# Kernel optimization log

Hardware: AMD Instinct MI355X
Metric: run time of the kernel (lower is better)

## Reference

```python
import jax, jax.numpy as jnp
import numpy as np

B, S, H, NH = 2, 2048, 2048, 16
HD = H // NH  # 128
NEG = -1e9


def _rope_tables(seq_len, dim, dtype):
    inv_freq = 1.0 / (10000.0 ** (jnp.arange(0, dim, 2, dtype=jnp.float32) / dim))
    t = jnp.arange(seq_len, dtype=jnp.float32)
    freqs = jnp.einsum('i,j->ij', t, inv_freq)          # [S, dim/2]
    emb = jnp.concatenate([freqs, freqs], axis=-1)      # [S, dim]
    return jnp.cos(emb).astype(dtype), jnp.sin(emb).astype(dtype)


def _rotate_half(x):
    x1, x2 = x[..., : x.shape[-1] // 2], x[..., x.shape[-1] // 2:]
    return jnp.concatenate([-x2, x1], axis=-1)


def setup_inputs() -> dict:
    key = jax.random.key(0)
    ks = jax.random.split(key, 5)
    hidden_states = jax.random.normal(ks[0], (B, S, H), dtype=jnp.float32)
    # causal additive mask [B, S, S]
    causal = jnp.where(jnp.tril(jnp.ones((S, S), dtype=bool)), 0.0, NEG).astype(jnp.float32)
    attention_mask = jnp.broadcast_to(causal, (B, S, S))
    sc = 1.0 / np.sqrt(H)
    Wq = jax.random.normal(ks[1], (H, H), dtype=jnp.float32) * sc
    Wk = jax.random.normal(ks[2], (H, H), dtype=jnp.float32) * sc
    Wv = jax.random.normal(ks[3], (H, H), dtype=jnp.float32) * sc
    Wo = jax.random.normal(ks[4], (H, H), dtype=jnp.float32) * sc
    return {"hidden_states": hidden_states, "attention_mask": attention_mask,
            "Wq": Wq, "Wk": Wk, "Wv": Wv, "Wo": Wo}


def reference(hidden_states, attention_mask, Wq, Wk, Wv, Wo):
    bsz, q_len, _ = hidden_states.shape
    dtype = hidden_states.dtype
    # QKV projections (nn.Linear: x @ W.T), split into heads -> [B, NH, S, HD]
    def proj(W):
        return jnp.einsum('bsh,dh->bsd', hidden_states, W).reshape(bsz, q_len, NH, HD).transpose(0, 2, 1, 3)
    q, k, v = proj(Wq), proj(Wk), proj(Wv)
    cos, sin = _rope_tables(q_len, HD, dtype)            # [S, HD]
    q = q * cos + _rotate_half(q) * sin
    k = k * cos + _rotate_half(k) * sin
    scaling = HD ** -0.5
    scores = jnp.einsum('bhqd,bhkd->bhqk', q, k) * scaling
    scores = scores + attention_mask[:, None, :, :]      # broadcast over heads
    attn = jax.nn.softmax(scores.astype(jnp.float32), axis=-1).astype(dtype)
    out = jnp.einsum('bhqk,bhkd->bhqd', attn, v)         # [B, NH, S, HD]
    out = out.transpose(0, 2, 1, 3).reshape(bsz, q_len, H)
    return jnp.einsum('bsh,dh->bsd', out, Wo)
```

## Files before the change

kernel.cpp:

```cpp
#include <hip/hip_runtime.h>
#include <hip/hip_bf16.h>
#include <math.h>

#define B_  2
#define S_  2048
#define H_  2048
#define NH_ 16
#define HD_ 128
#define M_  (B_*S_)

typedef __bf16 bf16_t;
typedef _Float16 f16_t;
typedef __bf16 bf16x8 __attribute__((ext_vector_type(8)));
typedef __bf16 bf16x4 __attribute__((ext_vector_type(4)));
typedef _Float16 f16x4 __attribute__((ext_vector_type(4)));
typedef float  f32x4  __attribute__((ext_vector_type(4)));

__device__ __forceinline__ f32x4 mfma_bf16_32(bf16x8 a, bf16x8 b, f32x4 c) {
  return __builtin_amdgcn_mfma_f32_16x16x32_bf16(a, b, c, 0, 0, 0);
}
__device__ __forceinline__ f32x4 mfma_f16_16(f16x4 a, f16x4 b, f32x4 c) {
  return __builtin_amdgcn_mfma_f32_16x16x16f16(a, b, c, 0, 0, 0);
}
__device__ __forceinline__ void gl_lds16(const void* g, void* l) {
  __builtin_amdgcn_global_load_lds((const __attribute__((address_space(1))) void*)g,
                                   (__attribute__((address_space(3))) void*)l, 16, 0, 0);
}
#define WAITCNT_VM(n) { asm volatile("" ::: "memory"); \
                        __builtin_amdgcn_s_waitcnt(((n) & 0xF) | 0x70 | 0xF00 | (((n) >> 4) << 14)); \
                        asm volatile("" ::: "memory"); }
#define BARRIER()     { asm volatile("" ::: "memory"); __builtin_amdgcn_s_barrier(); \
                        asm volatile("" ::: "memory"); }

__global__ void cvt_all(const float* __restrict__ hs, const float* __restrict__ wq,
                        const float* __restrict__ wk, const float* __restrict__ wv,
                        const float* __restrict__ wo, bf16_t* __restrict__ hs_b,
                        bf16_t* __restrict__ wqkv, bf16_t* __restrict__ wo_b) {
  int i = (blockIdx.x * 256 + threadIdx.x) * 4;
  const float* src;
  bf16_t* dst;
  if (i < 8388608)        { src = hs + i;              dst = hs_b + i; }
  else if (i < 12582912)  { src = wq + (i - 8388608);  dst = wqkv + (i - 8388608); }
  else if (i < 16777216)  { src = wk + (i - 12582912); dst = wqkv + (i - 8388608); }
  else if (i < 20971520)  { src = wv + (i - 16777216); dst = wqkv + (i - 8388608); }
  else                    { src = wo + (i - 20971520); dst = wo_b + (i - 20971520); }
  float4 v = *(const float4*)src;
  bf16x4 o;
  o[0] = (bf16_t)v.x; o[1] = (bf16_t)v.y; o[2] = (bf16_t)v.z; o[3] = (bf16_t)v.w;
  *(bf16x4*)dst = o;
}

template<int MODE>
__global__ __launch_bounds__(256, 3)
void gemm_mfma(const bf16_t* __restrict__ A, const bf16_t* __restrict__ Bt,
               bf16_t* __restrict__ outQ, bf16_t* __restrict__ outK,
               f16_t* __restrict__ outV, float* __restrict__ outF, int K) {
  __shared__ bf16_t sA[128 * 64];
  __shared__ bf16_t sB[128 * 64];
  const int tid  = threadIdx.x;
  const int lane = tid & 63;
  const int w    = tid >> 6;
  const int col  = lane & 15;
  const int quad = lane >> 4;
  const int w_m  = (w & 1) * 64;
  const int w_n2 = (w >> 1) * 32;
  const int m_blk = blockIdx.y * 128;
  const int n_blk = blockIdx.x * 128;

  const int srow   = lane >> 3;
  const int schunk = (lane & 7) ^ (lane >> 3);

  const bf16_t* Abase = A  + (size_t)m_blk * K;
  const bf16_t* Bbase = Bt + (size_t)n_blk * K;

  f32x4 acc[4][4] = {};

  for (int kk = 0; kk < K; kk += 64) {
    __syncthreads();
#pragma unroll
    for (int p = 0; p < 4; ++p) {
      int seg = w * 4 + p;
      int row = seg * 8 + srow;
      gl_lds16(Abase + (size_t)row * K + kk + schunk * 8, &sA[seg * 512]);
      gl_lds16(Bbase + (size_t)row * K + kk + schunk * 8, &sB[seg * 512]);
    }
    __syncthreads();
#pragma unroll
    for (int kc = 0; kc < 2; ++kc) {
      bf16x8 af[4], bfr[4];
      const int cs = (kc * 4 + quad) ^ (col & 7);
#pragma unroll
      for (int i = 0; i < 4; ++i) {
        af[i]  = *(const bf16x8*)&sA[(w_m + i * 16 + col) * 64 + cs * 8];
        bfr[i] = *(const bf16x8*)&sB[(w_n2 + (i & 1) * 16 + (i >> 1) * 64 + col) * 64 + cs * 8];
      }
#pragma unroll
      for (int mi = 0; mi < 4; ++mi)
#pragma unroll
        for (int ni = 0; ni < 4; ++ni)
          acc[mi][ni] = mfma_bf16_32(af[mi], bfr[ni], acc[mi][ni]);
    }
  }

  const int sel = n_blk >> 11;
  if (MODE == 0 && sel == 2) {
#pragma unroll
    for (int mi = 0; mi < 4; ++mi)
#pragma unroll
      for (int ni = 0; ni < 4; ++ni) {
        int m0 = m_blk + w_m + mi * 16 + quad * 4;
        int n  = n_blk + w_n2 + (ni & 1) * 16 + (ni >> 1) * 64 + col;
        int n_l = n & (H_ - 1);
        int head = n_l >> 7, hd = n_l & (HD_ - 1);
        int b = m0 >> 11, s0 = m0 & (S_ - 1);
        int bh = b * NH_ + head;
        int frag = (bh * 32 + (s0 >> 6)) * 32 + (hd >> 4) * 4 + ((s0 >> 4) & 3);
        int lane2 = ((s0 >> 2) & 3) * 16 + (hd & 15);
        f16x4 o;
#pragma unroll
        for (int r = 0; r < 4; ++r) o[r] = (f16_t)acc[mi][ni][r];
        *(f16x4*)&outV[(size_t)frag * 256 + lane2 * 4] = o;
      }
  } else if (MODE == 0) {
    const int head = (n_blk & (H_ - 1)) >> 7;
#pragma unroll
    for (int ni = 0; ni < 2; ++ni) {
      const int d = w_n2 + ni * 16 + col;
      const float rf = exp2f(-(float)d * 0.20762050593046f - 2.6514961294723187f);
#pragma unroll
      for (int mi = 0; mi < 4; ++mi) {
#pragma unroll
        for (int r = 0; r < 4; ++r) {
          int m = m_blk + w_m + mi * 16 + quad * 4 + r;
          int b = m >> 11, s = m & (S_ - 1);
          int bh = b * NH_ + head;
          float rev = (float)s * rf;
          rev -= floorf(rev);
          float cc = __builtin_amdgcn_cosf(rev);
          float sn = __builtin_amdgcn_sinf(rev);
          float x1 = acc[mi][ni][r], x2 = acc[mi][ni + 2][r];
          float o1 = x1 * cc - x2 * sn;
          float o2 = x2 * cc + x1 * sn;
          if (sel == 0) {
            bf16_t* qwr = outQ + ((size_t)bh * S_ + s) * HD_;
            qwr[d]      = (bf16_t)o1;
            qwr[d + 64] = (bf16_t)o2;
          } else {
            int kt = s >> 6, t = (s >> 4) & 3;
            int lane_ = ((d >> 3) & 3) * 16 + (s & 15);
            bf16_t* kbase = outK + ((size_t)(bh * 32 + kt) * 16) * 512;
            kbase[(size_t)(t * 4 + (d >> 5)) * 512 + lane_ * 8 + (d & 7)]     = (bf16_t)o1;
            kbase[(size_t)(t * 4 + (d >> 5) + 2) * 512 + lane_ * 8 + (d & 7)] = (bf16_t)o2;
          }
        }
      }
    }
  } else {
#pragma unroll
    for (int mi = 0; mi < 4; ++mi)
#pragma unroll
      for (int ni = 0; ni < 4; ++ni)
#pragma unroll
        for (int r = 0; r < 4; ++r) {
          int m = m_blk + w_m + mi * 16 + quad * 4 + r;
          int n = n_blk + w_n2 + (ni & 1) * 16 + (ni >> 1) * 64 + col;
          outF[(size_t)m * H_ + n] = acc[mi][ni][r];
        }
  }
}

__global__ __launch_bounds__(256, 4)
void flash_attn(const bf16_t* __restrict__ Q, const bf16_t* __restrict__ Kp,
                const f16_t* __restrict__ Vp, bf16_t* __restrict__ Out) {
  __shared__ bf16_t sK[8192];
  __shared__ f16_t  sV[8192];
  const int lane = threadIdx.x & 63;
  const int col  = lane & 15;
  const int quad = lane >> 4;
  const int w    = threadIdx.x >> 6;

  const int c = blockIdx.x & 7, g = blockIdx.x >> 3;
  const int g2 = (g + (blockIdx.y >> 3)) & 3;
  const int qt = (g2 == 0) ? c : (g2 == 1) ? 15 - c : (g2 == 2) ? 16 + c : 31 - c;
  const int bh = blockIdx.y;
  const int ktmax = qt;

  const bf16_t* KpB = Kp + (size_t)bh * 32 * 8192;
  const f16_t*  VpB = Vp + (size_t)bh * 32 * 8192;

  auto stageK = [&](int kt) {
#pragma unroll
    for (int r = 0; r < 4; ++r) {
      int seg = r * 4 + w;
      gl_lds16(KpB + (size_t)kt * 8192 + seg * 512 + lane * 8, &sK[seg * 512]);
    }
  };
  auto stageV = [&](int kt) {
#pragma unroll
    for (int r = 0; r < 4; ++r) {
      int seg = r * 4 + w;
      gl_lds16(VpB + (size_t)kt * 8192 + seg * 512 + lane * 8, &sV[seg * 512]);
    }
  };

  const float scale2 = 0.12751744154f;
  const bf16_t* Qrow = Q + ((size_t)bh * S_ + qt * 64 + w * 16 + col) * HD_;
  bf16x8 qf[4];
#pragma unroll
  for (int kc = 0; kc < 4; ++kc) {
    qf[kc] = *(const bf16x8*)(Qrow + kc * 32 + quad * 8);
#pragma unroll
    for (int j = 0; j < 8; ++j) qf[kc][j] = (bf16_t)((float)qf[kc][j] * scale2);
  }

  f32x4 oacc[8] = {};
  float m_i = -1e30f, l_i = 0.f;

  stageK(0);
  stageV(0);
  WAITCNT_VM(4)
  BARRIER();

  for (int kt = 0; kt <= ktmax; ++kt) {
    f32x4 st[4] = {};
    __builtin_amdgcn_s_setprio(1);
#pragma unroll
    for (int kc = 0; kc < 4; ++kc)
#pragma unroll
      for (int t = 0; t < 4; ++t) {
        bf16x8 kf = *(const bf16x8*)&sK[(t * 4 + kc) * 512 + lane * 8];
        st[t] = mfma_bf16_32(kf, qf[kc], st[t]);
      }
    __builtin_amdgcn_s_setprio(0);

    if (kt == ktmax) {
      int ql = w * 16 + col;
#pragma unroll
      for (int t = 0; t < 4; ++t)
#pragma unroll
        for (int r = 0; r < 4; ++r)
          if (t * 16 + quad * 4 + r > ql) st[t][r] = -1e30f;
    }

    float mx = st[0][0];
#pragma unroll
    for (int t = 0; t < 4; ++t)
#pragma unroll
      for (int r = 0; r < 4; ++r) mx = fmaxf(mx, st[t][r]);
    mx = fmaxf(mx, __shfl_xor(mx, 16, 64));
    mx = fmaxf(mx, __shfl_xor(mx, 32, 64));
    if (__ballot(mx - m_i > 8.0f)) {
      float mn = fmaxf(m_i, mx);
      float alpha = exp2f(m_i - mn);
#pragma unroll
      for (int dt = 0; dt < 8; ++dt)
#pragma unroll
        for (int r = 0; r < 4; ++r) oacc[dt][r] *= alpha;
      l_i *= alpha;
      m_i = mn;
    }

    float sum = 0.f;
    f16x4 pf[4];
#pragma unroll
    for (int t = 0; t < 4; ++t)
#pragma unroll
      for (int r = 0; r < 4; ++r) {
        float pv = exp2f(st[t][r] - m_i);
        sum += pv;
        pf[t][r] = (f16_t)pv;
      }
    sum += __shfl_xor(sum, 16, 64);
    sum += __shfl_xor(sum, 32, 64);
    l_i += sum;

    WAITCNT_VM(0)
    BARRIER();

    if (kt < ktmax) stageK(kt + 1);

    __builtin_amdgcn_s_setprio(1);
#pragma unroll
    for (int t = 0; t < 4; ++t)
#pragma unroll
      for (int dt = 0; dt < 8; ++dt) {
        f16x4 vf = *(const f16x4*)&sV[(dt * 4 + t) * 256 + lane * 4];
        oacc[dt] = mfma_f16_16(vf, pf[t], oacc[dt]);
      }
    __builtin_amdgcn_s_setprio(0);

    if (kt < ktmax) {
      BARRIER();
      stageV(kt + 1);
      WAITCNT_VM(4)
      BARRIER();
    }
  }

  float inv = 1.0f / l_i;
  int b = bh >> 4, h = bh & (NH_ - 1);
  int qg = qt * 64 + w * 16 + col;
  bf16_t* Orow = Out + ((size_t)b * S_ + qg) * H_ + h * HD_;
#pragma unroll
  for (int dt = 0; dt < 8; ++dt) {
    bf16x4 o4;
#pragma unroll
    for (int r = 0; r < 4; ++r) o4[r] = (bf16_t)(oacc[dt][r] * inv);
    *(bf16x4*)(Orow + dt * 16 + quad * 4) = o4;
  }
}

extern "C" void kernel_launch(void* const* d_in, const int* in_sizes, int n_in,
                              void* d_out, int out_size, void* d_ws, size_t ws_size,
                              hipStream_t stream) {
  const float* hs = (const float*)d_in[0];
  const float* Wq = (const float*)d_in[2];
  const float* Wk = (const float*)d_in[3];
  const float* Wv = (const float*)d_in[4];
  const float* Wo = (const float*)d_in[5];
  float* out = (float*)d_out;

  char* ws = (char*)d_ws;
  size_t off = 0;
  auto alloc = [&](size_t bytes) -> void* {
    void* p = ws + off;
    off += (bytes + 255) & ~(size_t)255;
    return p;
  };
  bf16_t* hs_b  = (bf16_t*)alloc((size_t)M_ * H_ * 2);
  bf16_t* wqkv  = (bf16_t*)alloc((size_t)3 * H_ * H_ * 2);
  bf16_t* wo_b  = (bf16_t*)alloc((size_t)H_ * H_ * 2);
  bf16_t* Qbuf  = (bf16_t*)alloc((size_t)M_ * H_ * 2);
  bf16_t* Kp    = (bf16_t*)alloc((size_t)M_ * H_ * 2);
  f16_t*  Vp    = (f16_t*)alloc((size_t)M_ * H_ * 2);
  bf16_t* attn  = (bf16_t*)alloc((size_t)M_ * H_ * 2);

  cvt_all<<<24576, 256, 0, stream>>>(hs, Wq, Wk, Wv, Wo, hs_b, wqkv, wo_b);

  gemm_mfma<0><<<dim3(48, 32), 256, 0, stream>>>(hs_b, wqkv, Qbuf, Kp,
                                                 Vp, nullptr, H_);

  flash_attn<<<dim3(32, 32), 256, 0, stream>>>(Qbuf, Kp, Vp, attn);

  gemm_mfma<1><<<dim3(16, 32), 256, 0, stream>>>(attn, wo_b, nullptr, nullptr,
                                                 nullptr, out, H_);
}
```

Before: 372.4 us.

## Double-buffer GEMM LDS tiles with 256x128 blocks and 8 waves

Reworks the projection GEMM into 512-thread blocks computing 256x128 tiles with double-buffered LDS. The next k-tile's global-to-LDS loads are issued before the MFMAs on the current tile, and s_setprio is raised around the MFMA bursts. The aim is to hide global load latency behind compute and reuse each B tile across more rows. In exchange it uses twice the LDS per block, adds extra barriers, and launches fewer blocks, which lowers occupancy.

Measured after the change: 387.0 us. 1.04x slower.

```diff
diff --git a/kernel.cpp b/kernel.cpp
--- a/kernel.cpp
+++ b/kernel.cpp
@@ -51,54 +51,89 @@
 }
 
 template<int MODE>
-__global__ __launch_bounds__(256, 3)
+__global__ __launch_bounds__(512, 2)
 void gemm_mfma(const bf16_t* __restrict__ A, const bf16_t* __restrict__ Bt,
                bf16_t* __restrict__ outQ, bf16_t* __restrict__ outK,
                f16_t* __restrict__ outV, float* __restrict__ outF, int K) {
-  __shared__ bf16_t sA[128 * 64];
-  __shared__ bf16_t sB[128 * 64];
+  __shared__ bf16_t sA[2][256 * 64];
+  __shared__ bf16_t sB[2][128 * 64];
   const int tid  = threadIdx.x;
   const int lane = tid & 63;
   const int w    = tid >> 6;
   const int col  = lane & 15;
   const int quad = lane >> 4;
-  const int w_m  = (w & 1) * 64;
-  const int w_n2 = (w >> 1) * 32;
-  const int m_blk = blockIdx.y * 128;
+  const int wr   = w >> 1;
+  const int wc   = w & 1;
+  const int m_blk = blockIdx.y * 256;
   const int n_blk = blockIdx.x * 128;
 
   const int srow   = lane >> 3;
-  const int schunk = (lane & 7) ^ (lane >> 3);
+  const int schunk = (lane & 7) ^ srow;
 
   const bf16_t* Abase = A  + (size_t)m_blk * K;
   const bf16_t* Bbase = Bt + (size_t)n_blk * K;
 
   f32x4 acc[4][4] = {};
 
-  for (int kk = 0; kk < K; kk += 64) {
-    __syncthreads();
-#pragma unroll
-    for (int p = 0; p < 4; ++p) {
-      int seg = w * 4 + p;
+  auto stage = [&](int kk, int p) {
+#pragma unroll
+    for (int q = 0; q < 4; ++q) {
+      int seg = w * 4 + q;
       int row = seg * 8 + srow;
-      gl_lds16(Abase + (size_t)row * K + kk + schunk * 8, &sA[seg * 512]);
-      gl_lds16(Bbase + (size_t)row * K + kk + schunk * 8, &sB[seg * 512]);
-    }
-    __syncthreads();
-#pragma unroll
-    for (int kc = 0; kc < 2; ++kc) {
+      gl_lds16(Abase + (size_t)row * K + kk + schunk * 8, &sA[p][seg * 512]);
+    }
+#pragma unroll
+    for (int q = 0; q < 2; ++q) {
+      int seg = w * 2 + q;
+      int row = seg * 8 + srow;
+      gl_lds16(Bbase + (size_t)row * K + kk + schunk * 8, &sB[p][seg * 512]);
+    }
+  };
+
+  stage(0, 0);
+  WAITCNT_VM(0)
+  BARRIER();
+
+  const int NT = K >> 6;
+  for (int t = 0; t < NT; ++t) {
+    const int cur = t & 1;
+    {
+      const int cs = quad ^ (col & 7);
       bf16x8 af[4], bfr[4];
-      const int cs = (kc * 4 + quad) ^ (col & 7);
 #pragma unroll
       for (int i = 0; i < 4; ++i) {
-        af[i]  = *(const bf16x8*)&sA[(w_m + i * 16 + col) * 64 + cs * 8];
-        bfr[i] = *(const bf16x8*)&sB[(w_n2 + (i & 1) * 16 + (i >> 1) * 64 + col) * 64 + cs * 8];
-      }
+        af[i]  = *(const bf16x8*)&sA[cur][(wr * 64 + i * 16 + col) * 64 + cs * 8];
+        bfr[i] = *(const bf16x8*)&sB[cur][(wc * 32 + (i & 1) * 16 + (i >> 1) * 64 + col) * 64 + cs * 8];
+      }
+      if (t + 1 < NT) stage((t + 1) << 6, cur ^ 1);
+      BARRIER();
+      __builtin_amdgcn_s_setprio(1);
 #pragma unroll
       for (int mi = 0; mi < 4; ++mi)
 #pragma unroll
         for (int ni = 0; ni < 4; ++ni)
           acc[mi][ni] = mfma_bf16_32(af[mi], bfr[ni], acc[mi][ni]);
+      __builtin_amdgcn_s_setprio(0);
+      BARRIER();
+    }
+    {
+      const int cs = (4 + quad) ^ (col & 7);
+      bf16x8 af[4], bfr[4];
+#pragma unroll
+      for (int i = 0; i < 4; ++i) {
+        af[i]  = *(const bf16x8*)&sA[cur][(wr * 64 + i * 16 + col) * 64 + cs * 8];
+        bfr[i] = *(const bf16x8*)&sB[cur][(wc * 32 + (i & 1) * 16 + (i >> 1) * 64 + col) * 64 + cs * 8];
+      }
+      BARRIER();
+      __builtin_amdgcn_s_setprio(1);
+#pragma unroll
+      for (int mi = 0; mi < 4; ++mi)
+#pragma unroll
+        for (int ni = 0; ni < 4; ++ni)
+          acc[mi][ni] = mfma_bf16_32(af[mi], bfr[ni], acc[mi][ni]);
+      __builtin_amdgcn_s_setprio(0);
+      WAITCNT_VM(0)
+      BARRIER();
     }
   }
 
@@ -108,8 +143,8 @@
     for (int mi = 0; mi < 4; ++mi)
 #pragma unroll
       for (int ni = 0; ni < 4; ++ni) {
-        int m0 = m_blk + w_m + mi * 16 + quad * 4;
-        int n  = n_blk + w_n2 + (ni & 1) * 16 + (ni >> 1) * 64 + col;
+        int m0 = m_blk + wr * 64 + mi * 16 + quad * 4;
+        int n  = n_blk + wc * 32 + (ni & 1) * 16 + (ni >> 1) * 64 + col;
         int n_l = n & (H_ - 1);
         int head = n_l >> 7, hd = n_l & (HD_ - 1);
         int b = m0 >> 11, s0 = m0 & (S_ - 1);
@@ -125,13 +160,13 @@
     const int head = (n_blk & (H_ - 1)) >> 7;
 #pragma unroll
     for (int ni = 0; ni < 2; ++ni) {
-      const int d = w_n2 + ni * 16 + col;
+      const int d = wc * 32 + ni * 16 + col;
       const float rf = exp2f(-(float)d * 0.20762050593046f - 2.6514961294723187f);
 #pragma unroll
       for (int mi = 0; mi < 4; ++mi) {
 #pragma unroll
         for (int r = 0; r < 4; ++r) {
-          int m = m_blk + w_m + mi * 16 + quad * 4 + r;
+          int m = m_blk + wr * 64 + mi * 16 + quad * 4 + r;
           int b = m >> 11, s = m & (S_ - 1);
           int bh = b * NH_ + head;
           float rev = (float)s * rf;
@@ -146,11 +181,11 @@
             qwr[d]      = (bf16_t)o1;
             qwr[d + 64] = (bf16_t)o2;
           } else {
-            int kt = s >> 6, t = (s >> 4) & 3;
+            int kt = s >> 6, t2 = (s >> 4) & 3;
             int lane_ = ((d >> 3) & 3) * 16 + (s & 15);
             bf16_t* kbase = outK + ((size_t)(bh * 32 + kt) * 16) * 512;
-            kbase[(size_t)(t * 4 + (d >> 5)) * 512 + lane_ * 8 + (d & 7)]     = (bf16_t)o1;
-            kbase[(size_t)(t * 4 + (d >> 5) + 2) * 512 + lane_ * 8 + (d & 7)] = (bf16_t)o2;
+            kbase[(size_t)(t2 * 4 + (d >> 5)) * 512 + lane_ * 8 + (d & 7)]     = (bf16_t)o1;
+            kbase[(size_t)(t2 * 4 + (d >> 5) + 2) * 512 + lane_ * 8 + (d & 7)] = (bf16_t)o2;
           }
         }
       }
@@ -162,8 +197,8 @@
       for (int ni = 0; ni < 4; ++ni)
 #pragma unroll
         for (int r = 0; r < 4; ++r) {
-          int m = m_blk + w_m + mi * 16 + quad * 4 + r;
-          int n = n_blk + w_n2 + (ni & 1) * 16 + (ni >> 1) * 64 + col;
+          int m = m_blk + wr * 64 + mi * 16 + quad * 4 + r;
+          int n = n_blk + wc * 32 + (ni & 1) * 16 + (ni >> 1) * 64 + col;
           outF[(size_t)m * H_ + n] = acc[mi][ni][r];
         }
   }
@@ -337,11 +372,11 @@
 
   cvt_all<<<24576, 256, 0, stream>>>(hs, Wq, Wk, Wv, Wo, hs_b, wqkv, wo_b);
 
-  gemm_mfma<0><<<dim3(48, 32), 256, 0, stream>>>(hs_b, wqkv, Qbuf, Kp,
+  gemm_mfma<0><<<dim3(48, 16), 512, 0, stream>>>(hs_b, wqkv, Qbuf, Kp,
                                                  Vp, nullptr, H_);
 
   flash_attn<<<dim3(32, 32), 256, 0, stream>>>(Qbuf, Kp, Vp, attn);
 
-  gemm_mfma<1><<<dim3(16, 32), 256, 0, stream>>>(attn, wo_b, nullptr, nullptr,
+  gemm_mfma<1><<<dim3(16, 16), 512, 0, stream>>>(attn, wo_b, nullptr, nullptr,
                                                  nullptr, out, H_);
 }
```
